# Kernel optimization log

Measured on AMD Instinct MI355X. Metric: run time of the kernel, lower is better.

Reference implementation:

```python
import jax, jax.numpy as jnp
import numpy as np

B, S, D, HD = 4, 4096, 1024, 64

def setup_inputs() -> dict:
    key = jax.random.key(0)
    ks = jax.random.split(key, 4)
    scale = 1.0 / np.sqrt(D)
    return {
        "x": jax.random.normal(ks[0], (B, S, D), dtype=jnp.float32),
        "wq": jax.random.normal(ks[1], (HD, D), dtype=jnp.float32) * scale,
        "bq": jnp.zeros((HD,), dtype=jnp.float32),
        "wk": jax.random.normal(ks[2], (HD, D), dtype=jnp.float32) * scale,
        "bk": jnp.zeros((HD,), dtype=jnp.float32),
        "wv": jax.random.normal(ks[3], (HD, D), dtype=jnp.float32) * scale,
        "bv": jnp.zeros((HD,), dtype=jnp.float32),
    }

def reference(x, wq, bq, wk, bk, wv, bv):
    seq_len = x.shape[1]
    head_dim = wq.shape[0]
    # projections: nn.Linear stores weight as [out, in]
    q = jnp.einsum('bsd,hd->bsh', x, wq) + bq  # [B,S,HD]
    k = jnp.einsum('bsd,hd->bsh', x, wk) + bk
    v = jnp.einsum('bsd,hd->bsh', x, wv) + bv
    score = jnp.einsum('bqh,bkh->bqk', q, k) / jnp.sqrt(jnp.float32(head_dim))  # [B,S,S]
    causal = jnp.tril(jnp.ones((seq_len, seq_len), dtype=bool))
    score = jnp.where(causal, score, -jnp.inf)
    attn = jax.nn.softmax(score, axis=-1)
    # dropout p=0.0 -> identity
    out = jnp.einsum('bqk,bkh->bqh', attn, v)  # [B,S,HD]
    return out
```

## Files before the change

kernel.cpp:

```cpp
#include <hip/hip_runtime.h>
#include <math.h>

#define B_   4
#define S_   4096
#define D_   1024
#define HD_  64

#define CK            8
#define CHUNKS_PER_B  288
#define FULL_CHUNKS   224
#define PSTRIDE       68
#define SLOT_F        (64 * PSTRIDE)

typedef float  f32x4  __attribute__((ext_vector_type(4)));
typedef __bf16 bf16x8 __attribute__((ext_vector_type(8)));

static __device__ __forceinline__ unsigned short f2bf(float f) {
    unsigned int u = __float_as_uint(f);
    u += 0x7FFFu + ((u >> 16) & 1u);
    return (unsigned short)(u >> 16);
}

static __device__ __forceinline__ int chunk_slot(int qi, int c) {
    const int a = qi >> 3, r = qi & 7;
    return qi + 4 * a * (a - 1) + a * r + c;
}

__global__ __launch_bounds__(256) void convert_w(
    const float* __restrict__ wq, const float* __restrict__ wk,
    const float* __restrict__ wv, unsigned short* __restrict__ wbf)
{
    const int col = blockIdx.x;
    const int p = col >> 6, h = col & 63;
    const float* src = (p == 0 ? wq : (p == 1 ? wk : wv)) + (size_t)h * D_;
    const int t = threadIdx.x;
    const float4 v = ((const float4*)src)[t];
    ushort4 o;
    o.x = f2bf(v.x); o.y = f2bf(v.y); o.z = f2bf(v.z); o.w = f2bf(v.w);
    *(ushort4*)&wbf[(size_t)col * D_ + 4 * t] = o;
}

__global__ __launch_bounds__(256) void proj_mfma(
    const float* __restrict__ x, const unsigned short* __restrict__ wbf,
    const float* __restrict__ bq, const float* __restrict__ bk,
    const float* __restrict__ bv,
    unsigned short* __restrict__ qbf, unsigned short* __restrict__ kbf,
    unsigned short* __restrict__ vtb)
{
    __shared__ unsigned short xs[32][136];
    __shared__ unsigned short wsh[96][136];

    const int t = threadIdx.x;
    const int w = t >> 6, lane = t & 63;
    const int n = lane & 15, g = lane >> 4;
    const int koff = 8 * g;
    const int rt = w & 1, cg = w >> 1;
    const size_t row0 = (size_t)blockIdx.x * 32;
    const int colbase = 96 * blockIdx.y;

    f32x4 acc[3];
#pragma unroll
    for (int i = 0; i < 3; ++i) acc[i] = (f32x4)0.f;

    for (int chunk = 0; chunk < 8; ++chunk) {
        const int d0 = chunk * 128;
        __syncthreads();
#pragma unroll
        for (int i = 0; i < 4; ++i) {
            int e = t + i * 256;
            int r = e >> 5, c4 = (e & 31) * 4;
            float4 v = *(const float4*)&x[(row0 + r) * D_ + d0 + c4];
            ushort4 o;
            o.x = f2bf(v.x); o.y = f2bf(v.y); o.z = f2bf(v.z); o.w = f2bf(v.w);
            *(ushort4*)&xs[r][c4] = o;
        }
#pragma unroll
        for (int i = 0; i < 6; ++i) {
            int e = t + i * 256;
            int col = e >> 4, g8 = (e & 15) * 8;
            uint4 v = *(const uint4*)&wbf[(size_t)(colbase + col) * D_ + d0 + g8];
            *(uint4*)&wsh[col][g8] = v;
        }
        __syncthreads();

#pragma unroll
        for (int ks = 0; ks < 4; ++ks) {
            const int k0 = 32 * ks;
            const bf16x8 a = *(const bf16x8*)&xs[16 * rt + n][k0 + koff];
#pragma unroll
            for (int ci = 0; ci < 3; ++ci) {
                const bf16x8 b = *(const bf16x8*)&wsh[48 * cg + 16 * ci + n][k0 + koff];
                acc[ci] = __builtin_amdgcn_mfma_f32_16x16x32_bf16(a, b, acc[ci], 0, 0, 0);
            }
        }
    }

#pragma unroll
    for (int ci = 0; ci < 3; ++ci) {
        const int gct = 6 * blockIdx.y + 3 * cg + ci;
        const int p = gct >> 2, h0 = (gct & 3) * 16;
        const int h = h0 + n;
        const float bb = (p == 0 ? bq : (p == 1 ? bk : bv))[h];
        if (p == 2) {
            const size_t grow0 = row0 + 16 * rt + 4 * g;
            const int bidx = (int)(grow0 >> 12);
            const int s0 = (int)(grow0 & 4095);
            ushort4 u;
            u.x = f2bf(acc[ci][0] + bb); u.y = f2bf(acc[ci][1] + bb);
            u.z = f2bf(acc[ci][2] + bb); u.w = f2bf(acc[ci][3] + bb);
            *(ushort4*)&vtb[((size_t)bidx * HD_ + h) * S_ + s0] = u;
        } else {
            unsigned short* outp = (p == 0 ? qbf : kbf);
            const float scale = (p == 0) ? 0.125f : 1.0f;
#pragma unroll
            for (int r = 0; r < 4; ++r) {
                const size_t grow = row0 + 16 * rt + 4 * g + r;
                outp[grow * HD_ + h] = f2bf((acc[ci][r] + bb) * scale);
            }
        }
    }
}

__global__ __launch_bounds__(256) void flash_splitk(
    const unsigned short* __restrict__ qg, const unsigned short* __restrict__ kg,
    const unsigned short* __restrict__ vt, float* __restrict__ out,
    float* __restrict__ part)
{
    __shared__ unsigned short qsh[64][72];
    __shared__ unsigned short ksh[64][72];
    __shared__ unsigned short vsh[64][72];
    __shared__ unsigned short psh[4][16][72];

    const int t    = threadIdx.x;
    const int w    = t >> 6;
    const int lane = t & 63;
    const int n    = lane & 15;
    const int g    = lane >> 4;
    const int koff = 8 * g;

    int b, qi, c;
    {
        const int idx = blockIdx.x;
        if (idx < B_ * FULL_CHUNKS) {
            b = idx / FULL_CHUNKS;
            int rem = idx - b * FULL_CHUNKS;
            qi = 8;
            while (rem >= (qi >> 3)) { rem -= (qi >> 3); ++qi; }
            c = rem;
        } else {
            const int r2 = idx - B_ * FULL_CHUNKS;
            b = r2 >> 6;
            qi = r2 & 63;
            c = qi >> 3;
        }
    }
    const int kt0 = c * CK;
    const int kt1 = min(qi, kt0 + CK - 1);
    const int nc  = (qi >> 3) + 1;

    const size_t qtile = ((size_t)b * S_ + (size_t)qi * 64) * HD_;

    {
        const uint4* src = (const uint4*)(qg + qtile);
#pragma unroll
        for (int i = 0; i < 2; ++i) {
            int e = t + i * 256;
            int r = e >> 3, gg = e & 7;
            *(uint4*)&qsh[r][8 * gg] = src[e];
        }
    }

    f32x4 o4[4];
#pragma unroll
    for (int i = 0; i < 4; ++i) o4[i] = (f32x4)0.f;
    float m_r = -INFINITY, l_r = 0.f;

    for (int kt = kt0; kt <= kt1; ++kt) {
        const size_t kvbase = ((size_t)b * S_ + (size_t)kt * 64) * HD_;
        __syncthreads();
        {
            const uint4* ksrc = (const uint4*)(kg + kvbase);
#pragma unroll
            for (int i = 0; i < 2; ++i) {
                int e = t + i * 256;
                int r = e >> 3, gg = e & 7;
                *(uint4*)&ksh[r][8 * gg] = ksrc[e];
            }
#pragma unroll
            for (int i = 0; i < 2; ++i) {
                int e = t + i * 256;
                int h = e >> 3, gg = e & 7;
                *(uint4*)&vsh[h][8 * gg] =
                    *(const uint4*)&vt[((size_t)b * HD_ + h) * S_ + kt * 64 + 8 * gg];
            }
        }
        __syncthreads();

        f32x4 sc[4];
#pragma unroll
        for (int mt = 0; mt < 4; ++mt) sc[mt] = (f32x4)0.f;
#pragma unroll
        for (int ks = 0; ks < 2; ++ks) {
            const bf16x8 bq8 = *(const bf16x8*)&qsh[16 * w + n][32 * ks + koff];
#pragma unroll
            for (int mt = 0; mt < 4; ++mt) {
                const bf16x8 ak = *(const bf16x8*)&ksh[16 * mt + n][32 * ks + koff];
                sc[mt] = __builtin_amdgcn_mfma_f32_16x16x32_bf16(ak, bq8, sc[mt], 0, 0, 0);
            }
        }

        if (kt == qi) {
            const int qloc = 16 * w + n;
#pragma unroll
            for (int mt = 0; mt < 4; ++mt)
#pragma unroll
                for (int r = 0; r < 4; ++r) {
                    const int kloc = 16 * mt + 4 * g + r;
                    if (kloc > qloc) sc[mt][r] = -INFINITY;
                }
        }

        float mx = -INFINITY;
#pragma unroll
        for (int mt = 0; mt < 4; ++mt)
#pragma unroll
            for (int r = 0; r < 4; ++r) mx = fmaxf(mx, sc[mt][r]);
        mx = fmaxf(mx, __shfl_xor(mx, 16));
        mx = fmaxf(mx, __shfl_xor(mx, 32));

        const float m_new = fmaxf(m_r, mx);
        const float alpha = __expf(m_r - m_new);
        float psum = 0.f;
#pragma unroll
        for (int mt = 0; mt < 4; ++mt)
#pragma unroll
            for (int r = 0; r < 4; ++r) {
                const float pe = __expf(sc[mt][r] - m_new);
                sc[mt][r] = pe;
                psum += pe;
            }
        psum += __shfl_xor(psum, 16);
        psum += __shfl_xor(psum, 32);
        l_r = l_r * alpha + psum;
        m_r = m_new;

#pragma unroll
        for (int ht = 0; ht < 4; ++ht)
#pragma unroll
            for (int r = 0; r < 4; ++r) o4[ht][r] *= alpha;

#pragma unroll
        for (int mt = 0; mt < 4; ++mt) {
            ushort4 u;
            u.x = f2bf(sc[mt][0]); u.y = f2bf(sc[mt][1]);
            u.z = f2bf(sc[mt][2]); u.w = f2bf(sc[mt][3]);
            *(ushort4*)&psh[w][n][16 * mt + 4 * g] = u;
        }

#pragma unroll
        for (int ks = 0; ks < 2; ++ks) {
            const bf16x8 ap = *(const bf16x8*)&psh[w][n][32 * ks + koff];
#pragma unroll
            for (int ht = 0; ht < 4; ++ht) {
                const bf16x8 av = *(const bf16x8*)&vsh[16 * ht + n][32 * ks + koff];
                o4[ht] = __builtin_amdgcn_mfma_f32_16x16x32_bf16(av, ap, o4[ht], 0, 0, 0);
            }
        }
    }

    const size_t qbase = ((size_t)b * S_ + (size_t)qi * 64) * HD_;
    if (nc == 1) {
        const float inv = 1.f / l_r;
        const size_t ob = qbase + (size_t)(16 * w + n) * HD_;
#pragma unroll
        for (int ht = 0; ht < 4; ++ht) {
            float4 rv;
            rv.x = o4[ht][0] * inv; rv.y = o4[ht][1] * inv;
            rv.z = o4[ht][2] * inv; rv.w = o4[ht][3] * inv;
            *(float4*)&out[ob + 16 * ht + 4 * g] = rv;
        }
    } else {
        const size_t sb = ((size_t)b * CHUNKS_PER_B + chunk_slot(qi, c)) * SLOT_F;
        const size_t pb = sb + (size_t)(16 * w + n) * PSTRIDE;
#pragma unroll
        for (int ht = 0; ht < 4; ++ht) {
            float4 rv;
            rv.x = o4[ht][0]; rv.y = o4[ht][1];
            rv.z = o4[ht][2]; rv.w = o4[ht][3];
            *(float4*)&part[pb + 16 * ht + 4 * g] = rv;
        }
        if (g == 0) {
            part[pb + 64] = m_r;
            part[pb + 65] = l_r;
        }
    }
}

__global__ __launch_bounds__(256) void combine(
    const float* __restrict__ part, float* __restrict__ out)
{
    const int t  = threadIdx.x;
    const int qr = t >> 2, tc = t & 3;
    const int qi = blockIdx.x + CK;
    const int b  = blockIdx.y;
    const int nc = (qi >> 3) + 1;

    const size_t base0 = ((size_t)b * CHUNKS_PER_B + chunk_slot(qi, 0)) * SLOT_F;

    float M = -INFINITY;
    for (int c0 = 0; c0 < nc; ++c0)
        M = fmaxf(M, part[base0 + (size_t)c0 * SLOT_F + qr * PSTRIDE + 64]);

    float L = 0.f;
    float o[16];
#pragma unroll
    for (int j = 0; j < 16; ++j) o[j] = 0.f;

    for (int c0 = 0; c0 < nc; ++c0) {
        const size_t sb = base0 + (size_t)c0 * SLOT_F + qr * PSTRIDE;
        const float m_c = part[sb + 64];
        const float l_c = part[sb + 65];
        const float w = __expf(m_c - M);
        L += w * l_c;
#pragma unroll
        for (int j = 0; j < 4; ++j) {
            const float4 ov = *(const float4*)&part[sb + tc * 16 + 4 * j];
            o[4 * j + 0] += w * ov.x; o[4 * j + 1] += w * ov.y;
            o[4 * j + 2] += w * ov.z; o[4 * j + 3] += w * ov.w;
        }
    }

    const float inv = 1.f / L;
    const size_t qbase = ((size_t)b * S_ + (size_t)qi * 64) * HD_;
#pragma unroll
    for (int j = 0; j < 4; ++j) {
        float4 r;
        r.x = o[4 * j + 0] * inv; r.y = o[4 * j + 1] * inv;
        r.z = o[4 * j + 2] * inv; r.w = o[4 * j + 3] * inv;
        *(float4*)&out[qbase + 16 * t + 4 * j] = r;
    }
}

extern "C" void kernel_launch(void* const* d_in, const int* in_sizes, int n_in,
                              void* d_out, int out_size, void* d_ws, size_t ws_size,
                              hipStream_t stream)
{
    const float* x  = (const float*)d_in[0];
    const float* wq = (const float*)d_in[1];
    const float* bq = (const float*)d_in[2];
    const float* wk = (const float*)d_in[3];
    const float* bk = (const float*)d_in[4];
    const float* wv = (const float*)d_in[5];
    const float* bv = (const float*)d_in[6];
    float* outp = (float*)d_out;

    const size_t n = (size_t)B_ * S_ * HD_;
    unsigned short* qbf = (unsigned short*)d_ws;
    unsigned short* kbf = qbf + n;
    unsigned short* vtb = kbf + n;
    unsigned short* wbf = vtb + n;
    float* part = (float*)(wbf + (size_t)192 * D_);

    convert_w<<<dim3(192), 256, 0, stream>>>(wq, wk, wv, wbf);
    proj_mfma<<<dim3(B_ * S_ / 32, 2), 256, 0, stream>>>(
        x, wbf, bq, bk, bv, qbf, kbf, vtb);
    flash_splitk<<<dim3(B_ * CHUNKS_PER_B), 256, 0, stream>>>(qbf, kbf, vtb, outp, part);
    combine<<<dim3(S_ / 64 - CK, B_), 256, 0, stream>>>(part, outp);
}
```

Baseline: 154.9 us.

## Fuse weight conversion into projection and combine into split-K flash via atomic counter

Removes the separate weight-conversion kernel by having the projection kernel load fp32 weights and convert to bf16 while staging into shared memory. Removes the separate combine kernel by having the last-finishing split-K block per query tile, detected through an atomic counter plus threadfences, perform the merge. This trades two kernel launches for a memset launch, redundant weight conversion across projection blocks, and a tail where the final block of each tile does the combine serially.

```diff
diff --git a/kernel.cpp b/kernel.cpp
--- a/kernel.cpp
+++ b/kernel.cpp
@@ -26,22 +26,10 @@
     return qi + 4 * a * (a - 1) + a * r + c;
 }
 
-__global__ __launch_bounds__(256) void convert_w(
+__global__ __launch_bounds__(256) void proj_mfma(
+    const float* __restrict__ x,
     const float* __restrict__ wq, const float* __restrict__ wk,
-    const float* __restrict__ wv, unsigned short* __restrict__ wbf)
-{
-    const int col = blockIdx.x;
-    const int p = col >> 6, h = col & 63;
-    const float* src = (p == 0 ? wq : (p == 1 ? wk : wv)) + (size_t)h * D_;
-    const int t = threadIdx.x;
-    const float4 v = ((const float4*)src)[t];
-    ushort4 o;
-    o.x = f2bf(v.x); o.y = f2bf(v.y); o.z = f2bf(v.z); o.w = f2bf(v.w);
-    *(ushort4*)&wbf[(size_t)col * D_ + 4 * t] = o;
-}
-
-__global__ __launch_bounds__(256) void proj_mfma(
-    const float* __restrict__ x, const unsigned short* __restrict__ wbf,
+    const float* __restrict__ wv,
     const float* __restrict__ bq, const float* __restrict__ bk,
     const float* __restrict__ bv,
     unsigned short* __restrict__ qbf, unsigned short* __restrict__ kbf,
@@ -75,11 +63,17 @@
             *(ushort4*)&xs[r][c4] = o;
         }
 #pragma unroll
-        for (int i = 0; i < 6; ++i) {
+        for (int i = 0; i < 12; ++i) {
             int e = t + i * 256;
-            int col = e >> 4, g8 = (e & 15) * 8;
-            uint4 v = *(const uint4*)&wbf[(size_t)(colbase + col) * D_ + d0 + g8];
-            *(uint4*)&wsh[col][g8] = v;
+            int col = e >> 5;
+            int c4 = (e & 31) * 4;
+            const int gcol = colbase + col;
+            const int p = gcol >> 6, h = gcol & 63;
+            const float* src = (p == 0 ? wq : (p == 1 ? wk : wv)) + (size_t)h * D_;
+            float4 v = *(const float4*)&src[d0 + c4];
+            ushort4 o;
+            o.x = f2bf(v.x); o.y = f2bf(v.y); o.z = f2bf(v.z); o.w = f2bf(v.w);
+            *(ushort4*)&wsh[col][c4] = o;
         }
         __syncthreads();
 
@@ -124,12 +118,13 @@
 __global__ __launch_bounds__(256) void flash_splitk(
     const unsigned short* __restrict__ qg, const unsigned short* __restrict__ kg,
     const unsigned short* __restrict__ vt, float* __restrict__ out,
-    float* __restrict__ part)
+    float* part, int* cnt)
 {
     __shared__ unsigned short qsh[64][72];
     __shared__ unsigned short ksh[64][72];
     __shared__ unsigned short vsh[64][72];
     __shared__ unsigned short psh[4][16][72];
+    __shared__ int isLast;
 
     const int t    = threadIdx.x;
     const int w    = t >> 6;
@@ -279,9 +274,12 @@
             rv.z = o4[ht][2] * inv; rv.w = o4[ht][3] * inv;
             *(float4*)&out[ob + 16 * ht + 4 * g] = rv;
         }
-    } else {
-        const size_t sb = ((size_t)b * CHUNKS_PER_B + chunk_slot(qi, c)) * SLOT_F;
-        const size_t pb = sb + (size_t)(16 * w + n) * PSTRIDE;
+        return;
+    }
+
+    const size_t base0 = ((size_t)b * CHUNKS_PER_B + chunk_slot(qi, 0)) * SLOT_F;
+    {
+        const size_t pb = base0 + (size_t)c * SLOT_F + (size_t)(16 * w + n) * PSTRIDE;
 #pragma unroll
         for (int ht = 0; ht < 4; ++ht) {
             float4 rv;
@@ -294,50 +292,49 @@
             part[pb + 65] = l_r;
         }
     }
-}
-
-__global__ __launch_bounds__(256) void combine(
-    const float* __restrict__ part, float* __restrict__ out)
-{
-    const int t  = threadIdx.x;
-    const int qr = t >> 2, tc = t & 3;
-    const int qi = blockIdx.x + CK;
-    const int b  = blockIdx.y;
-    const int nc = (qi >> 3) + 1;
-
-    const size_t base0 = ((size_t)b * CHUNKS_PER_B + chunk_slot(qi, 0)) * SLOT_F;
-
-    float M = -INFINITY;
-    for (int c0 = 0; c0 < nc; ++c0)
-        M = fmaxf(M, part[base0 + (size_t)c0 * SLOT_F + qr * PSTRIDE + 64]);
-
-    float L = 0.f;
-    float o[16];
-#pragma unroll
-    for (int j = 0; j < 16; ++j) o[j] = 0.f;
-
-    for (int c0 = 0; c0 < nc; ++c0) {
-        const size_t sb = base0 + (size_t)c0 * SLOT_F + qr * PSTRIDE;
-        const float m_c = part[sb + 64];
-        const float l_c = part[sb + 65];
-        const float w = __expf(m_c - M);
-        L += w * l_c;
+
+    __threadfence();
+    if (t == 0) {
+        const int old = atomicAdd(&cnt[b * 64 + qi], 1);
+        isLast = (old == nc - 1);
+    }
+    __syncthreads();
+    if (!isLast) return;
+    __threadfence();
+
+    {
+        const int qr = t >> 2, tc = t & 3;
+        float M = -INFINITY;
+        for (int c0 = 0; c0 < nc; ++c0)
+            M = fmaxf(M, part[base0 + (size_t)c0 * SLOT_F + qr * PSTRIDE + 64]);
+
+        float L = 0.f;
+        float o[16];
+#pragma unroll
+        for (int j = 0; j < 16; ++j) o[j] = 0.f;
+
+        for (int c0 = 0; c0 < nc; ++c0) {
+            const size_t sb = base0 + (size_t)c0 * SLOT_F + qr * PSTRIDE;
+            const float m_c = part[sb + 64];
+            const float l_c = part[sb + 65];
+            const float wgt = __expf(m_c - M);
+            L += wgt * l_c;
+#pragma unroll
+            for (int j = 0; j < 4; ++j) {
+                const float4 ov = *(const float4*)&part[sb + tc * 16 + 4 * j];
+                o[4 * j + 0] += wgt * ov.x; o[4 * j + 1] += wgt * ov.y;
+                o[4 * j + 2] += wgt * ov.z; o[4 * j + 3] += wgt * ov.w;
+            }
+        }
+
+        const float inv = 1.f / L;
 #pragma unroll
         for (int j = 0; j < 4; ++j) {
-            const float4 ov = *(const float4*)&part[sb + tc * 16 + 4 * j];
-            o[4 * j + 0] += w * ov.x; o[4 * j + 1] += w * ov.y;
-            o[4 * j + 2] += w * ov.z; o[4 * j + 3] += w * ov.w;
-        }
-    }
-
-    const float inv = 1.f / L;
-    const size_t qbase = ((size_t)b * S_ + (size_t)qi * 64) * HD_;
-#pragma unroll
-    for (int j = 0; j < 4; ++j) {
-        float4 r;
-        r.x = o[4 * j + 0] * inv; r.y = o[4 * j + 1] * inv;
-        r.z = o[4 * j + 2] * inv; r.w = o[4 * j + 3] * inv;
-        *(float4*)&out[qbase + 16 * t + 4 * j] = r;
+            float4 r;
+            r.x = o[4 * j + 0] * inv; r.y = o[4 * j + 1] * inv;
+            r.z = o[4 * j + 2] * inv; r.w = o[4 * j + 3] * inv;
+            *(float4*)&out[qbase + 16 * t + 4 * j] = r;
+        }
     }
 }
 
@@ -358,12 +355,12 @@
     unsigned short* qbf = (unsigned short*)d_ws;
     unsigned short* kbf = qbf + n;
     unsigned short* vtb = kbf + n;
-    unsigned short* wbf = vtb + n;
-    float* part = (float*)(wbf + (size_t)192 * D_);
-
-    convert_w<<<dim3(192), 256, 0, stream>>>(wq, wk, wv, wbf);
+    float* part = (float*)(vtb + n);
+    int* cnt = (int*)(part + (size_t)B_ * CHUNKS_PER_B * SLOT_F);
+
+    hipMemsetAsync(cnt, 0, (size_t)B_ * 64 * sizeof(int), stream);
     proj_mfma<<<dim3(B_ * S_ / 32, 2), 256, 0, stream>>>(
-        x, wbf, bq, bk, bv, qbf, kbf, vtb);
-    flash_splitk<<<dim3(B_ * CHUNKS_PER_B), 256, 0, stream>>>(qbf, kbf, vtb, outp, part);
-    combine<<<dim3(S_ / 64 - CK, B_), 256, 0, stream>>>(part, outp);
-}
+        x, wq, wk, wv, bq, bk, bv, qbf, kbf, vtb);
+    flash_splitk<<<dim3(B_ * CHUNKS_PER_B), 256, 0, stream>>>(
+        qbf, kbf, vtb, outp, part, cnt);
+}
```

After: 370.9 us. 2.39x slower.
